# Performance work log

Measured on AMD Instinct MI355X. Metric: run time of the kernel, lower is better.

Reference implementation:

```python
import jax, jax.numpy as jnp
import numpy as np

MARGIN = 1.0


def setup_inputs() -> dict:
    key = jax.random.key(0)
    k1, k2 = jax.random.split(key)
    B, D, C = 8192, 128, 128
    embeddings = jax.random.normal(k1, (B, D), dtype=jnp.float32)
    labels = jax.random.randint(k2, (B,), 0, C, dtype=jnp.int64)
    return {"embeddings": embeddings, "labels": labels}


def _pairwise_dist(x):
    # Euclidean cdist with a sqrt-safe-at-zero formulation (diag is exactly 0).
    sq = jnp.sum(x * x, axis=-1)
    d2 = jnp.maximum(sq[:, None] + sq[None, :] - 2.0 * (x @ x.T), 0.0)
    pos = d2 > 0
    return jnp.where(pos, jnp.sqrt(jnp.where(pos, d2, 1.0)), 0.0)


def reference(embeddings, labels):
    B = embeddings.shape[0]
    dist = _pairwise_dist(embeddings)  # [B, B]
    same = labels[:, None] == labels[None, :]  # [B, B]
    eye = jnp.eye(B, dtype=bool)
    is_pos = same & ~eye
    is_neg = ~same
    neg_inf = jnp.float32(-jnp.inf)
    pos_inf = jnp.float32(jnp.inf)
    hardest_pos = jnp.max(jnp.where(is_pos, dist, neg_inf), axis=1)  # [B]
    hardest_neg = jnp.min(jnp.where(is_neg, dist, pos_inf), axis=1)  # [B]
    valid = jnp.any(is_pos, axis=1) & jnp.any(is_neg, axis=1)
    per_row = jax.nn.relu(hardest_pos - hardest_neg + MARGIN)
    n_valid = jnp.sum(valid)
    loss = jnp.sum(jnp.where(valid, per_row, 0.0)) / jnp.maximum(n_valid, 1).astype(embeddings.dtype)
    # matches torch fallback of 0.0 when no valid anchors exist
    return jnp.where(n_valid > 0, loss, jnp.float32(0.0))
```

## Files before the change

kernel.cpp:

```cpp
#include <hip/hip_runtime.h>
#include <hip/hip_bf16.h>

typedef __attribute__((ext_vector_type(8))) short short8;
typedef __attribute__((ext_vector_type(4))) float floatx4;

#define B_ROWS 8192
#define DIM    128
#define NSPLIT 16
#define JSPAN  (B_ROWS / NSPLIT)
#define NTILE  (JSPAN / 16)
#define WAVES  4
#define RPW    64
#define BM     (WAVES * RPW)
#define NRB    (B_ROWS / BM)
#define BIAS   4096.0f


#define OFF_SQ   (2u << 20)
#define OFF_D2P  (OFF_SQ + (64u << 10))
#define OFF_D2N  (OFF_D2P + (512u << 10))
#define OFF_ACC  (OFF_D2N + (512u << 10))

__global__ __launch_bounds__(256) void prep_kernel(const float* __restrict__ x,
                                                   __hip_bfloat16* __restrict__ xf,
                                                   float* __restrict__ sq,
                                                   float* __restrict__ acc_sum,
                                                   int* __restrict__ done) {
    if (blockIdx.x == 0 && threadIdx.x == 0) { acc_sum[0] = 0.f; done[0] = 0; }
    const int row  = blockIdx.x * 4 + (threadIdx.x >> 6);
    const int lane = threadIdx.x & 63;
    const float2 v = *reinterpret_cast<const float2*>(x + row * DIM + lane * 2);
    __hip_bfloat162 b2;
    b2.x = __float2bfloat16(v.x);
    b2.y = __float2bfloat16(v.y);
    const int kk = lane >> 4;
    const int g  = (lane >> 2) & 3;
    const int e  = (lane & 3) * 2;
    const int idx = (row >> 4) * 2048 + kk * 512 + (g * 16 + (row & 15)) * 8 + e;
    *reinterpret_cast<__hip_bfloat162*>(xf + idx) = b2;
    float s = v.x * v.x + v.y * v.y;
    #pragma unroll
    for (int m = 1; m < 64; m <<= 1) s += __shfl_xor(s, m, 64);
    if (lane == 0) sq[row] = s;
}

__global__ __launch_bounds__(256, 2) void main_kernel(
    const __hip_bfloat16* __restrict__ xf,
    const float* __restrict__ sq,
    const int*  __restrict__ lab,
    float* __restrict__ d2p,
    float* __restrict__ d2n) {
    const int tid  = threadIdx.x;
    const int lane = tid & 63;
    const int wave = tid >> 6;
    const int l15  = lane & 15;
    const int g    = lane >> 4;
    const int rowbase = blockIdx.x * BM + wave * RPW;
    const int split   = blockIdx.y;
    const int jstart  = split * JSPAN;

    short8 a[4][4];
    #pragma unroll
    for (int s = 0; s < 4; ++s) {
        const __hip_bfloat16* ap = xf + ((size_t)(rowbase >> 4) + s) * 2048 + lane * 8;
        #pragma unroll
        for (int kk = 0; kk < 4; ++kk)
            a[s][kk] = *reinterpret_cast<const short8*>(ap + kk * 512);
    }
    int labi[4][4];
    #pragma unroll
    for (int s = 0; s < 4; ++s)
        #pragma unroll
        for (int q = 0; q < 4; ++q)
            labi[s][q] = lab[rowbase + s * 16 + g * 4 + q];

    float mx[4][4], mn[4][4];
    #pragma unroll
    for (int s = 0; s < 4; ++s)
        #pragma unroll
        for (int q = 0; q < 4; ++q) { mx[s][q] = -INFINITY; mn[s][q] = INFINITY; }

    const __hip_bfloat16* bbase = xf + (size_t)(jstart >> 4) * 2048 + lane * 8;

    short8 bA[4], bB[4];
    float sqA, sqB; int labA, labB;
    #pragma unroll
    for (int kk = 0; kk < 4; ++kk) {
        bA[kk] = *reinterpret_cast<const short8*>(bbase + kk * 512);
        bB[kk] = *reinterpret_cast<const short8*>(bbase + 2048 + kk * 512);
    }
    sqA  = sq[jstart + l15];          labA = lab[jstart + l15];
    sqB  = sq[jstart + 16 + l15];     labB = lab[jstart + 16 + l15];

    float tA[4][4], tB[4][4];

    #define MFMA_TILE(BB, T, SQJ, LABJ)                                         \
    do {                                                                        \
        floatx4 acc[4];                                                         \
        _Pragma("unroll")                                                       \
        for (int s = 0; s < 4; ++s) acc[s] = (floatx4){0.f, 0.f, 0.f, 0.f};     \
        _Pragma("unroll")                                                       \
        for (int kk = 0; kk < 4; ++kk) {                                        \
            _Pragma("unroll")                                                   \
            for (int s = 0; s < 4; ++s)                                         \
                acc[s] = __builtin_amdgcn_mfma_f32_16x16x32_bf16(a[s][kk], BB[kk], acc[s], 0, 0, 0); \
        }                                                                       \
        const float sqjb = (SQJ) + BIAS;                                        \
        _Pragma("unroll")                                                       \
        for (int s = 0; s < 4; ++s) {                                           \
            _Pragma("unroll")                                                   \
            for (int q = 0; q < 4; ++q)                                         \
                T[s][q] = fmaf(-2.f, acc[s][q], ((LABJ) == labi[s][q]) ? sqjb : (SQJ)); \
        }                                                                       \
    } while (0)

    for (int jt = 0; jt < NTILE; jt += 2) {
        MFMA_TILE(bA, tA, sqA, labA);
        if (jt + 2 < NTILE) {
            const __hip_bfloat16* bp = bbase + (size_t)(jt + 2) * 2048;
            #pragma unroll
            for (int kk = 0; kk < 4; ++kk)
                bA[kk] = *reinterpret_cast<const short8*>(bp + kk * 512);
            sqA  = sq[jstart + (jt + 2) * 16 + l15];
            labA = lab[jstart + (jt + 2) * 16 + l15];
        }
        MFMA_TILE(bB, tB, sqB, labB);
        if (jt + 3 < NTILE) {
            const __hip_bfloat16* bp = bbase + (size_t)(jt + 3) * 2048;
            #pragma unroll
            for (int kk = 0; kk < 4; ++kk)
                bB[kk] = *reinterpret_cast<const short8*>(bp + kk * 512);
            sqB  = sq[jstart + (jt + 3) * 16 + l15];
            labB = lab[jstart + (jt + 3) * 16 + l15];
        }
        #pragma unroll
        for (int s = 0; s < 4; ++s)
            #pragma unroll
            for (int q = 0; q < 4; ++q) {
                mx[s][q] = fmaxf(fmaxf(mx[s][q], tA[s][q]), tB[s][q]);
                mn[s][q] = fminf(fminf(mn[s][q], tA[s][q]), tB[s][q]);
            }
    }
    #undef MFMA_TILE

    #pragma unroll
    for (int s = 0; s < 4; ++s)
        #pragma unroll
        for (int q = 0; q < 4; ++q) {
            #pragma unroll
            for (int mk = 1; mk < 16; mk <<= 1) {
                mx[s][q] = fmaxf(mx[s][q], __shfl_xor(mx[s][q], mk, 64));
                mn[s][q] = fminf(mn[s][q], __shfl_xor(mn[s][q], mk, 64));
            }
        }
    if (l15 == 0) {
        #pragma unroll
        for (int s = 0; s < 4; ++s)
            #pragma unroll
            for (int q = 0; q < 4; ++q) {
                const int i = rowbase + s * 16 + g * 4 + q;
                const float sqi = sq[i];
                d2p[split * B_ROWS + i] = sqi + (mx[s][q] - BIAS);
                d2n[split * B_ROWS + i] = sqi + mn[s][q];
            }
    }
}

__global__ __launch_bounds__(256) void combine_kernel(
    const float* __restrict__ d2p, const float* __restrict__ d2n,
    float* __restrict__ acc_sum, int* __restrict__ done,
    float* __restrict__ out) {
    const int row = blockIdx.x * 256 + threadIdx.x;
    float p = -INFINITY, n = INFINITY;
    #pragma unroll
    for (int s = 0; s < NSPLIT; ++s) {
        p = fmaxf(p, d2p[s * B_ROWS + row]);
        n = fminf(n, d2n[s * B_ROWS + row]);
    }
    float v = fmaxf(sqrtf(fmaxf(p, 0.f)) - sqrtf(fmaxf(n, 0.f)) + 1.0f, 0.f);
    #pragma unroll
    for (int mk = 1; mk < 64; mk <<= 1) v += __shfl_xor(v, mk, 64);
    __shared__ float sv[4];
    const int wv = threadIdx.x >> 6;
    if ((threadIdx.x & 63) == 0) sv[wv] = v;
    __syncthreads();
    if (threadIdx.x == 0) {
        atomicAdd(acc_sum, sv[0] + sv[1] + sv[2] + sv[3]);
        __threadfence();
        const int old = atomicAdd(done, 1);
        if (old == (int)gridDim.x - 1) {
            const float fs = atomicAdd(acc_sum, 0.f);
            out[0] = fs / (float)B_ROWS;
        }
    }
}

extern "C" void kernel_launch(void* const* d_in, const int* in_sizes, int n_in,
                              void* d_out, int out_size, void* d_ws, size_t ws_size,
                              hipStream_t stream) {
    const float* x   = (const float*)d_in[0];
    const int*   lab = (const int*)d_in[1];
    float*       out = (float*)d_out;

    char* ws = (char*)d_ws;
    __hip_bfloat16* xf = (__hip_bfloat16*)ws;
    float* sq      = (float*)(ws + OFF_SQ);
    float* d2p     = (float*)(ws + OFF_D2P);
    float* d2n     = (float*)(ws + OFF_D2N);
    float* acc_sum = (float*)(ws + OFF_ACC);
    int*   done    = (int*)(ws + OFF_ACC + 4);

    prep_kernel<<<B_ROWS / 4, 256, 0, stream>>>(x, xf, sq, acc_sum, done);
    main_kernel<<<dim3(NRB, NSPLIT), 256, 0, stream>>>(xf, sq, lab, d2p, d2n);
    combine_kernel<<<B_ROWS / 256, 256, 0, stream>>>(d2p, d2n, acc_sum, done, out);
}
```

Baseline: 34.66 us.

## Stage B tiles through LDS with async global_load_lds quad-buffered pipeline

Replaces per-wave register-prefetched global loads of the column (B) tiles with a block-shared, four-deep LDS ring filled by global_load_lds. All four waves now share one copy of each B tile instead of each loading it separately. Squared norms and labels are packed into one float2 array in the prep kernel and preloaded into LDS. The cost is a barrier and a vmcnt wait on every tile iteration, plus LDS usage that may limit occupancy.

New measurement: 43.08 us. 24.3% more time.

```diff
diff --git a/kernel.cpp b/kernel.cpp
--- a/kernel.cpp
+++ b/kernel.cpp
@@ -3,6 +3,7 @@
 
 typedef __attribute__((ext_vector_type(8))) short short8;
 typedef __attribute__((ext_vector_type(4))) float floatx4;
+typedef __attribute__((ext_vector_type(2))) float floatx2;
 
 #define B_ROWS 8192
 #define DIM    128
@@ -16,14 +17,21 @@
 #define BIAS   4096.0f
 
 
-#define OFF_SQ   (2u << 20)
-#define OFF_D2P  (OFF_SQ + (64u << 10))
-#define OFF_D2N  (OFF_D2P + (512u << 10))
-#define OFF_ACC  (OFF_D2N + (512u << 10))
+#define OFF_SQ    (2u << 20)
+#define OFF_SQLAB (OFF_SQ + (64u << 10))
+#define OFF_D2P   (OFF_SQLAB + (64u << 10))
+#define OFF_D2N   (OFF_D2P + (512u << 10))
+#define OFF_ACC   (OFF_D2N + (512u << 10))
+
+#define GLOAD_LDS(g, l) __builtin_amdgcn_global_load_lds(                     \
+    (const __attribute__((address_space(1))) void*)(g),                       \
+    (__attribute__((address_space(3))) void*)(l), 16, 0, 0)
 
 __global__ __launch_bounds__(256) void prep_kernel(const float* __restrict__ x,
+                                                   const int* __restrict__ lab,
                                                    __hip_bfloat16* __restrict__ xf,
                                                    float* __restrict__ sq,
+                                                   float2* __restrict__ sqlab,
                                                    float* __restrict__ acc_sum,
                                                    int* __restrict__ done) {
     if (blockIdx.x == 0 && threadIdx.x == 0) { acc_sum[0] = 0.f; done[0] = 0; }
@@ -41,15 +49,23 @@
     float s = v.x * v.x + v.y * v.y;
     #pragma unroll
     for (int m = 1; m < 64; m <<= 1) s += __shfl_xor(s, m, 64);
-    if (lane == 0) sq[row] = s;
+    if (lane == 0) {
+        sq[row] = s;
+        float2 p; p.x = s; p.y = __int_as_float(lab[row]);
+        sqlab[row] = p;
+    }
 }
 
 __global__ __launch_bounds__(256, 2) void main_kernel(
     const __hip_bfloat16* __restrict__ xf,
     const float* __restrict__ sq,
     const int*  __restrict__ lab,
+    const float2* __restrict__ sqlab,
     float* __restrict__ d2p,
     float* __restrict__ d2n) {
+    __shared__ __align__(16) char ldsT[4][4096];
+    __shared__ __align__(16) char ldsS[4096];
+
     const int tid  = threadIdx.x;
     const int lane = tid & 63;
     const int wave = tid >> 6;
@@ -59,6 +75,15 @@
     const int split   = blockIdx.y;
     const int jstart  = split * JSPAN;
 
+    {
+        const char* gs = (const char*)sqlab + (size_t)jstart * 8;
+        GLOAD_LDS(gs + tid * 16, &ldsS[wave * 1024]);
+        const char* gt = (const char*)xf + (size_t)(jstart >> 4) * 4096;
+        GLOAD_LDS(gt +      tid * 16, &ldsT[0][wave * 1024]);
+        GLOAD_LDS(gt + 4096 + tid * 16, &ldsT[1][wave * 1024]);
+        GLOAD_LDS(gt + 8192 + tid * 16, &ldsT[2][wave * 1024]);
+    }
+
     short8 a[4][4];
     #pragma unroll
     for (int s = 0; s < 4; ++s) {
@@ -80,68 +105,47 @@
         #pragma unroll
         for (int q = 0; q < 4; ++q) { mx[s][q] = -INFINITY; mn[s][q] = INFINITY; }
 
-    const __hip_bfloat16* bbase = xf + (size_t)(jstart >> 4) * 2048 + lane * 8;
-
-    short8 bA[4], bB[4];
-    float sqA, sqB; int labA, labB;
-    #pragma unroll
-    for (int kk = 0; kk < 4; ++kk) {
-        bA[kk] = *reinterpret_cast<const short8*>(bbase + kk * 512);
-        bB[kk] = *reinterpret_cast<const short8*>(bbase + 2048 + kk * 512);
-    }
-    sqA  = sq[jstart + l15];          labA = lab[jstart + l15];
-    sqB  = sq[jstart + 16 + l15];     labB = lab[jstart + 16 + l15];
-
-    float tA[4][4], tB[4][4];
-
-    #define MFMA_TILE(BB, T, SQJ, LABJ)                                         \
-    do {                                                                        \
-        floatx4 acc[4];                                                         \
-        _Pragma("unroll")                                                       \
-        for (int s = 0; s < 4; ++s) acc[s] = (floatx4){0.f, 0.f, 0.f, 0.f};     \
-        _Pragma("unroll")                                                       \
-        for (int kk = 0; kk < 4; ++kk) {                                        \
-            _Pragma("unroll")                                                   \
-            for (int s = 0; s < 4; ++s)                                         \
-                acc[s] = __builtin_amdgcn_mfma_f32_16x16x32_bf16(a[s][kk], BB[kk], acc[s], 0, 0, 0); \
-        }                                                                       \
-        const float sqjb = (SQJ) + BIAS;                                        \
-        _Pragma("unroll")                                                       \
-        for (int s = 0; s < 4; ++s) {                                           \
-            _Pragma("unroll")                                                   \
-            for (int q = 0; q < 4; ++q)                                         \
-                T[s][q] = fmaf(-2.f, acc[s][q], ((LABJ) == labi[s][q]) ? sqjb : (SQJ)); \
-        }                                                                       \
-    } while (0)
-
-    for (int jt = 0; jt < NTILE; jt += 2) {
-        MFMA_TILE(bA, tA, sqA, labA);
-        if (jt + 2 < NTILE) {
-            const __hip_bfloat16* bp = bbase + (size_t)(jt + 2) * 2048;
-            #pragma unroll
-            for (int kk = 0; kk < 4; ++kk)
-                bA[kk] = *reinterpret_cast<const short8*>(bp + kk * 512);
-            sqA  = sq[jstart + (jt + 2) * 16 + l15];
-            labA = lab[jstart + (jt + 2) * 16 + l15];
-        }
-        MFMA_TILE(bB, tB, sqB, labB);
-        if (jt + 3 < NTILE) {
-            const __hip_bfloat16* bp = bbase + (size_t)(jt + 3) * 2048;
-            #pragma unroll
-            for (int kk = 0; kk < 4; ++kk)
-                bB[kk] = *reinterpret_cast<const short8*>(bp + kk * 512);
-            sqB  = sq[jstart + (jt + 3) * 16 + l15];
-            labB = lab[jstart + (jt + 3) * 16 + l15];
-        }
-        #pragma unroll
-        for (int s = 0; s < 4; ++s)
+    #define STAGE(buf_, tile_) GLOAD_LDS(                                     \
+        (const char*)xf + ((size_t)(jstart >> 4) + (unsigned)(tile_)) * 4096  \
+            + tid * 16,                                                       \
+        &ldsT[buf_][wave * 1024])
+
+    for (int jt = 0; jt < NTILE; ++jt) {
+        asm volatile("s_waitcnt vmcnt(2)" ::: "memory");
+        __builtin_amdgcn_s_barrier();
+        STAGE((jt + 3) & 3, (jt + 3) & 31);
+
+        const int buf = jt & 3;
+        short8 b[4];
+        #pragma unroll
+        for (int kk = 0; kk < 4; ++kk)
+            b[kk] = *reinterpret_cast<const short8*>(&ldsT[buf][kk * 1024 + lane * 16]);
+        const floatx2 sl = *reinterpret_cast<const floatx2*>(&ldsS[(jt * 16 + l15) * 8]);
+        const float sqj  = sl[0];
+        const int   labj = __float_as_int(sl[1]);
+
+        floatx4 acc[4];
+        #pragma unroll
+        for (int s = 0; s < 4; ++s) acc[s] = (floatx4){0.f, 0.f, 0.f, 0.f};
+        #pragma unroll
+        for (int kk = 0; kk < 4; ++kk) {
+            #pragma unroll
+            for (int s = 0; s < 4; ++s)
+                acc[s] = __builtin_amdgcn_mfma_f32_16x16x32_bf16(a[s][kk], b[kk], acc[s], 0, 0, 0);
+        }
+
+        const float sqjb = sqj + BIAS;
+        #pragma unroll
+        for (int s = 0; s < 4; ++s) {
             #pragma unroll
             for (int q = 0; q < 4; ++q) {
-                mx[s][q] = fmaxf(fmaxf(mx[s][q], tA[s][q]), tB[s][q]);
-                mn[s][q] = fminf(fminf(mn[s][q], tA[s][q]), tB[s][q]);
+                const float t = fmaf(-2.f, acc[s][q], (labj == labi[s][q]) ? sqjb : sqj);
+                mx[s][q] = fmaxf(mx[s][q], t);
+                mn[s][q] = fminf(mn[s][q], t);
             }
-    }
-    #undef MFMA_TILE
+        }
+    }
+    #undef STAGE
 
     #pragma unroll
     for (int s = 0; s < 4; ++s)
@@ -204,13 +208,14 @@
 
     char* ws = (char*)d_ws;
     __hip_bfloat16* xf = (__hip_bfloat16*)ws;
-    float* sq      = (float*)(ws + OFF_SQ);
-    float* d2p     = (float*)(ws + OFF_D2P);
-    float* d2n     = (float*)(ws + OFF_D2N);
-    float* acc_sum = (float*)(ws + OFF_ACC);
-    int*   done    = (int*)(ws + OFF_ACC + 4);
-
-    prep_kernel<<<B_ROWS / 4, 256, 0, stream>>>(x, xf, sq, acc_sum, done);
-    main_kernel<<<dim3(NRB, NSPLIT), 256, 0, stream>>>(xf, sq, lab, d2p, d2n);
+    float*  sq      = (float*)(ws + OFF_SQ);
+    float2* sqlab   = (float2*)(ws + OFF_SQLAB);
+    float*  d2p     = (float*)(ws + OFF_D2P);
+    float*  d2n     = (float*)(ws + OFF_D2N);
+    float*  acc_sum = (float*)(ws + OFF_ACC);
+    int*    done    = (int*)(ws + OFF_ACC + 4);
+
+    prep_kernel<<<B_ROWS / 4, 256, 0, stream>>>(x, lab, xf, sq, sqlab, acc_sum, done);
+    main_kernel<<<dim3(NRB, NSPLIT), 256, 0, stream>>>(xf, sq, lab, sqlab, d2p, d2n);
     combine_kernel<<<B_ROWS / 256, 256, 0, stream>>>(d2p, d2n, acc_sum, done, out);
 }
```

## Deepen B-tile prefetch, fuse min/max, atomically reduce splits, vectorize prep

Applied to the files above, without the earlier changes.

The main loop now keeps four B tiles in flight instead of two and folds each tile's distances straight into the running max/min, with no temporary tile arrays. The per-split partial results are no longer written to global buffers for the combine kernel to reduce. Instead, main_kernel merges them with integer atomicMax/atomicMin on float bit patterns, made order-preserving by a positive offset. The prep kernel is restructured so each lane converts eight floats with vector loads and writes a whole short8, using fewer blocks. The costs are more registers, which may hurt occupancy under launch_bounds(256,2), atomic contention across the 16 splits, and correctness that depends on the offset keeping every value positive.

After: 44.01 us. +27.0%, slower.

```diff
diff --git a/kernel.cpp b/kernel.cpp
--- a/kernel.cpp
+++ b/kernel.cpp
@@ -14,42 +14,64 @@
 #define BM     (WAVES * RPW)
 #define NRB    (B_ROWS / BM)
 #define BIAS   4096.0f
-
-
-#define OFF_SQ   (2u << 20)
-#define OFF_D2P  (OFF_SQ + (64u << 10))
-#define OFF_D2N  (OFF_D2P + (512u << 10))
-#define OFF_ACC  (OFF_D2N + (512u << 10))
+#define KOFF   64.0f
+
+
+#define OFF_SQ  (2u << 20)
+#define OFF_KP  (OFF_SQ + (64u << 10))
+#define OFF_KN  (OFF_KP + (32u << 10))
+#define OFF_ACC (OFF_KN + (32u << 10))
 
 __global__ __launch_bounds__(256) void prep_kernel(const float* __restrict__ x,
                                                    __hip_bfloat16* __restrict__ xf,
                                                    float* __restrict__ sq,
+                                                   int* __restrict__ kp,
+                                                   int* __restrict__ kn,
                                                    float* __restrict__ acc_sum,
                                                    int* __restrict__ done) {
-    if (blockIdx.x == 0 && threadIdx.x == 0) { acc_sum[0] = 0.f; done[0] = 0; }
-    const int row  = blockIdx.x * 4 + (threadIdx.x >> 6);
-    const int lane = threadIdx.x & 63;
-    const float2 v = *reinterpret_cast<const float2*>(x + row * DIM + lane * 2);
-    __hip_bfloat162 b2;
-    b2.x = __float2bfloat16(v.x);
-    b2.y = __float2bfloat16(v.y);
-    const int kk = lane >> 4;
-    const int g  = (lane >> 2) & 3;
-    const int e  = (lane & 3) * 2;
-    const int idx = (row >> 4) * 2048 + kk * 512 + (g * 16 + (row & 15)) * 8 + e;
-    *reinterpret_cast<__hip_bfloat162*>(xf + idx) = b2;
-    float s = v.x * v.x + v.y * v.y;
-    #pragma unroll
-    for (int m = 1; m < 64; m <<= 1) s += __shfl_xor(s, m, 64);
-    if (lane == 0) sq[row] = s;
+    const int tid = threadIdx.x;
+    const int gid = blockIdx.x * 256 + tid;
+    if (gid < B_ROWS) { kp[gid] = 0; kn[gid] = 0x7F7F7F7F; }
+    if (gid == 0) { acc_sum[0] = 0.f; done[0] = 0; }
+
+    const int wv   = tid >> 6;
+    const int lane = tid & 63;
+    const int t    = blockIdx.x * 4 + wv;
+    const int row  = t * 16 + (lane & 15);
+    const float* xp = x + (size_t)row * DIM + (lane >> 4) * 8;
+
+    float s = 0.f;
+    #pragma unroll
+    for (int kk = 0; kk < 4; ++kk) {
+        const float4 v0 = *reinterpret_cast<const float4*>(xp + kk * 32);
+        const float4 v1 = *reinterpret_cast<const float4*>(xp + kk * 32 + 4);
+        short8 o;
+        {
+            __hip_bfloat16 h;
+            h = __float2bfloat16(v0.x); o[0] = *reinterpret_cast<short*>(&h);
+            h = __float2bfloat16(v0.y); o[1] = *reinterpret_cast<short*>(&h);
+            h = __float2bfloat16(v0.z); o[2] = *reinterpret_cast<short*>(&h);
+            h = __float2bfloat16(v0.w); o[3] = *reinterpret_cast<short*>(&h);
+            h = __float2bfloat16(v1.x); o[4] = *reinterpret_cast<short*>(&h);
+            h = __float2bfloat16(v1.y); o[5] = *reinterpret_cast<short*>(&h);
+            h = __float2bfloat16(v1.z); o[6] = *reinterpret_cast<short*>(&h);
+            h = __float2bfloat16(v1.w); o[7] = *reinterpret_cast<short*>(&h);
+        }
+        *reinterpret_cast<short8*>(xf + (size_t)t * 2048 + kk * 512 + lane * 8) = o;
+        s += v0.x * v0.x + v0.y * v0.y + v0.z * v0.z + v0.w * v0.w
+           + v1.x * v1.x + v1.y * v1.y + v1.z * v1.z + v1.w * v1.w;
+    }
+    s += __shfl_xor(s, 16, 64);
+    s += __shfl_xor(s, 32, 64);
+    if (lane < 16) sq[row] = s;
 }
 
 __global__ __launch_bounds__(256, 2) void main_kernel(
     const __hip_bfloat16* __restrict__ xf,
     const float* __restrict__ sq,
     const int*  __restrict__ lab,
-    float* __restrict__ d2p,
-    float* __restrict__ d2n) {
+    int* __restrict__ kp,
+    int* __restrict__ kn) {
     const int tid  = threadIdx.x;
     const int lane = tid & 63;
     const int wave = tid >> 6;
@@ -82,66 +104,57 @@
 
     const __hip_bfloat16* bbase = xf + (size_t)(jstart >> 4) * 2048 + lane * 8;
 
-    short8 bA[4], bB[4];
-    float sqA, sqB; int labA, labB;
-    #pragma unroll
-    for (int kk = 0; kk < 4; ++kk) {
-        bA[kk] = *reinterpret_cast<const short8*>(bbase + kk * 512);
-        bB[kk] = *reinterpret_cast<const short8*>(bbase + 2048 + kk * 512);
-    }
-    sqA  = sq[jstart + l15];          labA = lab[jstart + l15];
-    sqB  = sq[jstart + 16 + l15];     labB = lab[jstart + 16 + l15];
-
-    float tA[4][4], tB[4][4];
-
-    #define MFMA_TILE(BB, T, SQJ, LABJ)                                         \
-    do {                                                                        \
-        floatx4 acc[4];                                                         \
-        _Pragma("unroll")                                                       \
-        for (int s = 0; s < 4; ++s) acc[s] = (floatx4){0.f, 0.f, 0.f, 0.f};     \
-        _Pragma("unroll")                                                       \
-        for (int kk = 0; kk < 4; ++kk) {                                        \
-            _Pragma("unroll")                                                   \
-            for (int s = 0; s < 4; ++s)                                         \
+    short8 b0[4], b1[4], b2[4], b3[4];
+    float sq0, sq1, sq2, sq3;
+    int   lb0, lb1, lb2, lb3;
+
+    #define LOADT(BB, SQ, LB, T)                                               \
+    do {                                                                       \
+        const __hip_bfloat16* bp_ = bbase + (size_t)(T) * 2048;                \
+        _Pragma("unroll")                                                      \
+        for (int kk = 0; kk < 4; ++kk)                                         \
+            BB[kk] = *reinterpret_cast<const short8*>(bp_ + kk * 512);         \
+        SQ = sq[jstart + (T) * 16 + l15];                                      \
+        LB = lab[jstart + (T) * 16 + l15];                                     \
+    } while (0)
+
+    #define STEP(BB, SQJ, LABJ)                                                \
+    do {                                                                       \
+        floatx4 acc[4];                                                        \
+        _Pragma("unroll")                                                      \
+        for (int s = 0; s < 4; ++s) acc[s] = (floatx4){0.f, 0.f, 0.f, 0.f};    \
+        _Pragma("unroll")                                                      \
+        for (int kk = 0; kk < 4; ++kk) {                                       \
+            _Pragma("unroll")                                                  \
+            for (int s = 0; s < 4; ++s)                                        \
                 acc[s] = __builtin_amdgcn_mfma_f32_16x16x32_bf16(a[s][kk], BB[kk], acc[s], 0, 0, 0); \
-        }                                                                       \
-        const float sqjb = (SQJ) + BIAS;                                        \
-        _Pragma("unroll")                                                       \
-        for (int s = 0; s < 4; ++s) {                                           \
-            _Pragma("unroll")                                                   \
-            for (int q = 0; q < 4; ++q)                                         \
-                T[s][q] = fmaf(-2.f, acc[s][q], ((LABJ) == labi[s][q]) ? sqjb : (SQJ)); \
-        }                                                                       \
+        }                                                                      \
+        const float sqjb_ = (SQJ) + BIAS;                                      \
+        _Pragma("unroll")                                                      \
+        for (int s = 0; s < 4; ++s) {                                          \
+            _Pragma("unroll")                                                  \
+            for (int q = 0; q < 4; ++q) {                                      \
+                const float t_ = fmaf(-2.f, acc[s][q],                         \
+                                      ((LABJ) == labi[s][q]) ? sqjb_ : (SQJ)); \
+                mx[s][q] = fmaxf(mx[s][q], t_);                                \
+                mn[s][q] = fminf(mn[s][q], t_);                                \
+            }                                                                  \
+        }                                                                      \
     } while (0)
 
-    for (int jt = 0; jt < NTILE; jt += 2) {
-        MFMA_TILE(bA, tA, sqA, labA);
-        if (jt + 2 < NTILE) {
-            const __hip_bfloat16* bp = bbase + (size_t)(jt + 2) * 2048;
-            #pragma unroll
-            for (int kk = 0; kk < 4; ++kk)
-                bA[kk] = *reinterpret_cast<const short8*>(bp + kk * 512);
-            sqA  = sq[jstart + (jt + 2) * 16 + l15];
-            labA = lab[jstart + (jt + 2) * 16 + l15];
-        }
-        MFMA_TILE(bB, tB, sqB, labB);
-        if (jt + 3 < NTILE) {
-            const __hip_bfloat16* bp = bbase + (size_t)(jt + 3) * 2048;
-            #pragma unroll
-            for (int kk = 0; kk < 4; ++kk)
-                bB[kk] = *reinterpret_cast<const short8*>(bp + kk * 512);
-            sqB  = sq[jstart + (jt + 3) * 16 + l15];
-            labB = lab[jstart + (jt + 3) * 16 + l15];
-        }
-        #pragma unroll
-        for (int s = 0; s < 4; ++s)
-            #pragma unroll
-            for (int q = 0; q < 4; ++q) {
-                mx[s][q] = fmaxf(fmaxf(mx[s][q], tA[s][q]), tB[s][q]);
-                mn[s][q] = fminf(fminf(mn[s][q], tA[s][q]), tB[s][q]);
-            }
-    }
-    #undef MFMA_TILE
+    LOADT(b0, sq0, lb0, 0);
+    LOADT(b1, sq1, lb1, 1);
+    LOADT(b2, sq2, lb2, 2);
+    LOADT(b3, sq3, lb3, 3);
+
+    for (int jt = 0; jt < NTILE; jt += 4) {
+        STEP(b0, sq0, lb0); if (jt + 4 < NTILE) LOADT(b0, sq0, lb0, jt + 4);
+        STEP(b1, sq1, lb1); if (jt + 5 < NTILE) LOADT(b1, sq1, lb1, jt + 5);
+        STEP(b2, sq2, lb2); if (jt + 6 < NTILE) LOADT(b2, sq2, lb2, jt + 6);
+        STEP(b3, sq3, lb3); if (jt + 7 < NTILE) LOADT(b3, sq3, lb3, jt + 7);
+    }
+    #undef STEP
+    #undef LOADT
 
     #pragma unroll
     for (int s = 0; s < 4; ++s)
@@ -160,24 +173,22 @@
             for (int q = 0; q < 4; ++q) {
                 const int i = rowbase + s * 16 + g * 4 + q;
                 const float sqi = sq[i];
-                d2p[split * B_ROWS + i] = sqi + (mx[s][q] - BIAS);
-                d2n[split * B_ROWS + i] = sqi + mn[s][q];
+                const float kpv = sqi + mx[s][q] + KOFF;
+                const float knv = sqi + mn[s][q] + KOFF;
+                atomicMax(&kp[i], __float_as_int(kpv));
+                atomicMin(&kn[i], __float_as_int(knv));
             }
     }
 }
 
 __global__ __launch_bounds__(256) void combine_kernel(
-    const float* __restrict__ d2p, const float* __restrict__ d2n,
+    const int* __restrict__ kp, const int* __restrict__ kn,
     float* __restrict__ acc_sum, int* __restrict__ done,
     float* __restrict__ out) {
     const int row = blockIdx.x * 256 + threadIdx.x;
-    float p = -INFINITY, n = INFINITY;
-    #pragma unroll
-    for (int s = 0; s < NSPLIT; ++s) {
-        p = fmaxf(p, d2p[s * B_ROWS + row]);
-        n = fminf(n, d2n[s * B_ROWS + row]);
-    }
-    float v = fmaxf(sqrtf(fmaxf(p, 0.f)) - sqrtf(fmaxf(n, 0.f)) + 1.0f, 0.f);
+    const float hp2 = __int_as_float(kp[row]) - BIAS - KOFF;
+    const float hn2 = __int_as_float(kn[row]) - KOFF;
+    float v = fmaxf(sqrtf(fmaxf(hp2, 0.f)) - sqrtf(fmaxf(hn2, 0.f)) + 1.0f, 0.f);
     #pragma unroll
     for (int mk = 1; mk < 64; mk <<= 1) v += __shfl_xor(v, mk, 64);
     __shared__ float sv[4];
@@ -205,12 +216,12 @@
     char* ws = (char*)d_ws;
     __hip_bfloat16* xf = (__hip_bfloat16*)ws;
     float* sq      = (float*)(ws + OFF_SQ);
-    float* d2p     = (float*)(ws + OFF_D2P);
-    float* d2n     = (float*)(ws + OFF_D2N);
+    int*   kp      = (int*)(ws + OFF_KP);
+    int*   kn      = (int*)(ws + OFF_KN);
     float* acc_sum = (float*)(ws + OFF_ACC);
     int*   done    = (int*)(ws + OFF_ACC + 4);
 
-    prep_kernel<<<B_ROWS / 4, 256, 0, stream>>>(x, xf, sq, acc_sum, done);
-    main_kernel<<<dim3(NRB, NSPLIT), 256, 0, stream>>>(xf, sq, lab, d2p, d2n);
-    combine_kernel<<<B_ROWS / 256, 256, 0, stream>>>(d2p, d2n, acc_sum, done, out);
-}
+    prep_kernel<<<B_ROWS / 64, 256, 0, stream>>>(x, xf, sq, kp, kn, acc_sum, done);
+    main_kernel<<<dim3(NRB, NSPLIT), 256, 0, stream>>>(xf, sq, lab, kp, kn);
+    combine_kernel<<<B_ROWS / 256, 256, 0, stream>>>(kp, kn, acc_sum, done, out);
+}
```
